# Kernel tuning notes

Hardware: AMD Instinct MI355X
Metric: run time of the kernel (lower is better)

The kernel has to match this reference:

```python
import jax, jax.numpy as jnp
import numpy as np

N_DIMS = 4
NEG_SLOPE = 0.01
ALPHA = 0.5

def leaky(v):
    return jnp.where(v > 0, v, NEG_SLOPE * v)

def gcn_conv(h, W, b, edge_index, n):
    """PyG GCNConv: add self-loops, symmetric normalization, then aggregate."""
    hw = h @ W  # [N, H]
    loops = jnp.arange(n, dtype=edge_index.dtype)
    src = jnp.concatenate([edge_index[0], loops])
    dst = jnp.concatenate([edge_index[1], loops])
    deg = jax.ops.segment_sum(jnp.ones_like(dst, dtype=hw.dtype), dst, num_segments=n)
    dinv = jnp.where(deg > 0, jax.lax.rsqrt(deg), 0.0)
    norm = dinv[src] * dinv[dst]  # [E+N]
    out = jax.ops.segment_sum(hw[src] * norm[:, None], dst, num_segments=n)
    return out + b

def setup_inputs() -> dict:
    key = jax.random.key(0)
    ks = jax.random.split(key, 8)
    N, IN, H, OUT, E = 50000, 512, 256, 512, 800000
    def kaiming(k, shape, fan_in):
        bound = np.sqrt(6.0 / fan_in)  # kaiming_uniform a=sqrt(5)-ish approx; gain sqrt(2)/sqrt(fan_in)*sqrt(3)
        bound = np.sqrt(2.0) * np.sqrt(3.0 / fan_in)
        return jax.random.uniform(k, shape, jnp.float32, -bound, bound)
    x = jax.random.normal(ks[0], (N, IN), jnp.float32)
    all_dim_edge_index = jax.random.randint(ks[1], (N_DIMS, 2, E), 0, N, jnp.int64)
    proj_mat = kaiming(ks[2], (N_DIMS, IN, H), IN)
    gcn_W = jax.random.uniform(ks[3], (N_DIMS, H, H), jnp.float32, -1, 1) * np.sqrt(1.0 / H)
    gcn_b = jnp.zeros((N_DIMS, H), jnp.float32)
    bilinear = kaiming(ks[4], (H, H), H)
    fan = H * N_DIMS
    inv_W = jax.random.uniform(ks[5], (fan, OUT), jnp.float32, -np.sqrt(1.0 / fan), np.sqrt(1.0 / fan))
    inv_b = jax.random.uniform(ks[6], (OUT,), jnp.float32, -np.sqrt(1.0 / fan), np.sqrt(1.0 / fan))
    return {"x": x, "all_dim_edge_index": all_dim_edge_index, "proj_mat": proj_mat,
            "gcn_W": gcn_W, "gcn_b": gcn_b, "bilinear": bilinear, "inv_W": inv_W, "inv_b": inv_b}

def reference(x, all_dim_edge_index, proj_mat, gcn_W, gcn_b, bilinear, inv_W, inv_b):
    n = x.shape[0]
    # per-dimension projection: [n_dims, N, H]
    dim_repr = leaky(jnp.einsum('ni,dih->dnh', x, proj_mat))
    # within-dimension GCN message passing (loop over small fixed n_dims)
    within_aggr = jnp.stack([
        gcn_conv(dim_repr[d], gcn_W[d], gcn_b[d], all_dim_edge_index[d], n)
        for d in range(N_DIMS)])
    # cross-dimension attention
    attention = jnp.einsum('aji,ik,bjk->ab', proj_mat, bilinear, proj_mat)
    attention = jax.nn.softmax(attention, axis=0)
    across_aggr = jnp.einsum('ab,anh->bnh', attention, dim_repr)
    new_dim_repr = ALPHA * within_aggr + (1.0 - ALPHA) * across_aggr  # [n_dims, N, H]
    concat = jnp.transpose(new_dim_repr, (1, 0, 2)).reshape(n, -1)  # [N, n_dims*H]
    return leaky(concat @ inv_W + inv_b)
```

## Files before the change

### kernel.cpp

```cpp
#include <hip/hip_runtime.h>
#include <math.h>

constexpr int N_NODES = 50000;
constexpr int IN_F    = 512;
constexpr int H_F     = 256;
constexpr int OUT_F   = 512;
constexpr int N_EDGE  = 800000;
constexpr int NDIM    = 4;
constexpr long NH     = (long)N_NODES * H_F;

#define LEAKY_SLOPE 0.01f

__device__ __forceinline__ float leaky_f(float v) { return v > 0.0f ? v : LEAKY_SLOPE * v; }

typedef __bf16 bf16x8 __attribute__((ext_vector_type(8)));
typedef float  f32x4  __attribute__((ext_vector_type(4)));

__global__ __launch_bounds__(256) void mfma_gemm_kernel(
    const float* __restrict__ A1, const float* __restrict__ A2, int kSplit,
    const __bf16* __restrict__ BhT, const __bf16* __restrict__ BlT,
    float* __restrict__ C,
    int M, int N, int K, int lda1, int lda2, int ldc,
    int accumulate, int leaky)
{
  __shared__ __bf16 Ash[128][40];
  __shared__ __bf16 Asl[128][40];
  __shared__ __bf16 Bsh[128][40];
  __shared__ __bf16 Bsl[128][40];

  const int tid  = threadIdx.x;
  const int wid  = tid >> 6;
  const int lane = tid & 63;
  const int wm   = wid & 1;
  const int wn   = wid >> 1;
  const int row0 = blockIdx.x * 128;
  const int col0 = blockIdx.y * 128;
  const int l15  = lane & 15;
  const int quad = lane >> 4;

  const int sAm = tid >> 3;
  const int sAk = (tid & 7) * 4;
  const int sBn = tid >> 2;
  const int sBk = (tid & 3) * 8;

  f32x4 acc[4][4] = {};

  const int nkt = K >> 5;
  for (int kt = 0; kt < nkt; ++kt) {
    const float* Asrc; int lda; int k0;
    if (kt * 32 < kSplit) { Asrc = A1; lda = lda1; k0 = kt * 32; }
    else                  { Asrc = A2; lda = lda2; k0 = kt * 32 - kSplit; }

    __syncthreads();
    #pragma unroll
    for (int p = 0; p < 4; ++p) {
      int m = sAm + p * 32;
      int row = row0 + m;
      row = row < M ? row : M - 1;
      float4 v = *(const float4*)(Asrc + (long)row * lda + k0 + sAk);
      float f[4] = {v.x, v.y, v.z, v.w};
      union { __bf16 b[4]; short4 s; } h, l;
      #pragma unroll
      for (int i = 0; i < 4; ++i) {
        __bf16 hb = (__bf16)f[i];
        h.b[i] = hb;
        l.b[i] = (__bf16)(f[i] - (float)hb);
      }
      *(short4*)&Ash[m][sAk] = h.s;
      *(short4*)&Asl[m][sAk] = l.s;
    }
    #pragma unroll
    for (int p = 0; p < 2; ++p) {
      int n = sBn + p * 64;
      long off = (long)(col0 + n) * K + kt * 32 + sBk;
      *(int4*)&Bsh[n][sBk] = *(const int4*)(BhT + off);
      *(int4*)&Bsl[n][sBk] = *(const int4*)(BlT + off);
    }
    __syncthreads();

    bf16x8 ah[4], al[4], bh[4], bl[4];
    #pragma unroll
    for (int t = 0; t < 4; ++t) {
      ah[t] = *(const bf16x8*)&Ash[wm * 64 + t * 16 + l15][quad * 8];
      al[t] = *(const bf16x8*)&Asl[wm * 64 + t * 16 + l15][quad * 8];
      bh[t] = *(const bf16x8*)&Bsh[wn * 64 + t * 16 + l15][quad * 8];
      bl[t] = *(const bf16x8*)&Bsl[wn * 64 + t * 16 + l15][quad * 8];
    }
    #pragma unroll
    for (int mt = 0; mt < 4; ++mt)
      #pragma unroll
      for (int nt = 0; nt < 4; ++nt) {
        acc[mt][nt] = __builtin_amdgcn_mfma_f32_16x16x32_bf16(ah[mt], bh[nt], acc[mt][nt], 0, 0, 0);
        acc[mt][nt] = __builtin_amdgcn_mfma_f32_16x16x32_bf16(ah[mt], bl[nt], acc[mt][nt], 0, 0, 0);
        acc[mt][nt] = __builtin_amdgcn_mfma_f32_16x16x32_bf16(al[mt], bh[nt], acc[mt][nt], 0, 0, 0);
      }
  }

  #pragma unroll
  for (int mt = 0; mt < 4; ++mt)
    #pragma unroll
    for (int nt = 0; nt < 4; ++nt) {
      int col = col0 + wn * 64 + nt * 16 + l15;
      #pragma unroll
      for (int r = 0; r < 4; ++r) {
        int row = row0 + wm * 64 + mt * 16 + quad * 4 + r;
        if (row < M) {
          float* cp = C + (long)row * ldc + col;
          float v = acc[mt][nt][r];
          if (accumulate) v += *cp;
          if (leaky) v = leaky_f(v);
          *cp = v;
        }
      }
    }
}

__global__ __launch_bounds__(256) void sgemm_kernel(
    const float* __restrict__ A, const float* __restrict__ B, float* __restrict__ C,
    int M, int N, int K, int lda, int ldb, int ldc)
{
  __shared__ float As[16][68];
  __shared__ float Bs[16][68];
  const int tid = threadIdx.x;
  const int tx  = tid & 15;
  const int ty  = tid >> 4;
  const int row0 = blockIdx.x * 64;
  const int col0 = blockIdx.y * 64;
  const int mA = tid >> 2;
  const int kA = (tid & 3) * 4;
  const int kB = tid >> 4;
  const int nB = (tid & 15) * 4;
  const int  rowA   = row0 + mA;
  const bool aValid = rowA < M;
  const long aRowOff = (long)rowA * lda;
  float acc[4][4] = {};
  for (int k0 = 0; k0 < K; k0 += 16) {
    float4 av = make_float4(0.f, 0.f, 0.f, 0.f);
    if (aValid) av = *(const float4*)(A + aRowOff + k0 + kA);
    As[kA + 0][mA] = av.x; As[kA + 1][mA] = av.y;
    As[kA + 2][mA] = av.z; As[kA + 3][mA] = av.w;
    float4 bv = *(const float4*)(B + (long)(k0 + kB) * ldb + col0 + nB);
    *(float4*)&Bs[kB][nB] = bv;
    __syncthreads();
    #pragma unroll
    for (int k = 0; k < 16; ++k) {
      float4 a4 = *(const float4*)&As[k][ty * 4];
      float4 b4 = *(const float4*)&Bs[k][tx * 4];
      float ar[4] = {a4.x, a4.y, a4.z, a4.w};
      float br[4] = {b4.x, b4.y, b4.z, b4.w};
      #pragma unroll
      for (int i = 0; i < 4; ++i)
        #pragma unroll
        for (int j = 0; j < 4; ++j)
          acc[i][j] = fmaf(ar[i], br[j], acc[i][j]);
    }
    __syncthreads();
  }
  #pragma unroll
  for (int i = 0; i < 4; ++i) {
    int r = row0 + ty * 4 + i;
    if (r < M)
      *(float4*)(C + (long)r * ldc + col0 + tx * 4) =
          make_float4(acc[i][0], acc[i][1], acc[i][2], acc[i][3]);
  }
}

__global__ void splitT_kernel(const float* __restrict__ B, __bf16* __restrict__ h,
                              __bf16* __restrict__ l, int Kd, int Nd, int total)
{
  int i = blockIdx.x * 256 + threadIdx.x;
  if (i >= total) return;
  int z   = i / (Kd * Nd);
  int rem = i - z * (Kd * Nd);
  int k = rem / Nd;
  int n = rem - k * Nd;
  float v = B[i];
  __bf16 hv = (__bf16)v;
  long o = (long)z * Kd * Nd + (long)n * Kd + k;
  h[o] = hv;
  l[o] = (__bf16)(v - (float)hv);
}

__global__ void bcat_kernel(const float* __restrict__ invW, const float* __restrict__ att,
                            __bf16* __restrict__ h, __bf16* __restrict__ l)
{
  int i = blockIdx.x * 256 + threadIdx.x;
  if (i >= NDIM * OUT_F * 512) return;
  int d   = i >> 18;
  int rem = i & 262143;
  int n = rem >> 9;
  int k = rem & 511;
  float v;
  if (k < H_F) {
    v = invW[(long)(d * H_F + k) * OUT_F + n];
  } else {
    float s = 0.f;
    #pragma unroll
    for (int b = 0; b < 4; ++b)
      s += att[d * 4 + b] * invW[(long)(b * H_F + (k - H_F)) * OUT_F + n];
    v = 0.5f * s;
  }
  __bf16 hv = (__bf16)v;
  h[i] = hv;
  l[i] = (__bf16)(v - (float)hv);
}

__global__ void deg_count_kernel(const int* __restrict__ edges, int* __restrict__ cnt, int E)
{
  int i = blockIdx.x * 256 + threadIdx.x;
  if (i >= NDIM * E) return;
  int d = i / E;
  int e = i - d * E;
  int t = edges[(long)d * 2 * E + E + e];
  atomicAdd(&cnt[d * N_NODES + t], 1);
}

__global__ __launch_bounds__(1024) void scan_kernel(const int* __restrict__ cnt,
                                                    int* __restrict__ row_start,
                                                    float* __restrict__ dinv)
{
  const int d    = blockIdx.x;
  const int tid  = threadIdx.x;
  const int lane = tid & 63;
  const int wid  = tid >> 6;
  __shared__ int wsum[16];
  __shared__ int carry_s;
  if (tid == 0) carry_s = 0;
  __syncthreads();
  for (int base = 0; base < N_NODES; base += 1024) {
    int i = base + tid;
    int v = (i < N_NODES) ? cnt[d * N_NODES + i] : 0;
    if (i < N_NODES) dinv[d * N_NODES + i] = sqrtf(0.5f / (float)(v + 1));
    int incl = v;
    #pragma unroll
    for (int off = 1; off < 64; off <<= 1) {
      int nb = __shfl_up(incl, off, 64);
      if (lane >= off) incl += nb;
    }
    if (lane == 63) wsum[wid] = incl;
    __syncthreads();
    if (wid == 0 && lane < 16) {
      int s = wsum[lane];
      #pragma unroll
      for (int off = 1; off < 16; off <<= 1) {
        int nb = __shfl_up(s, off, 16);
        if (lane >= off) s += nb;
      }
      wsum[lane] = s;
    }
    __syncthreads();
    int waveoff = (wid == 0) ? 0 : wsum[wid - 1];
    if (i < N_NODES) row_start[d * (N_NODES + 1) + i] = carry_s + waveoff + incl - v;
    __syncthreads();
    if (tid == 1023) carry_s += wsum[15];
    __syncthreads();
  }
  if (tid == 0) row_start[d * (N_NODES + 1) + N_NODES] = carry_s;
}

__global__ void fill_kernel(const int* __restrict__ edges, const int* __restrict__ row_start,
                            int* __restrict__ fill_cnt, int* __restrict__ csr_src, int E)
{
  int i = blockIdx.x * 256 + threadIdx.x;
  if (i >= NDIM * E) return;
  int d = i / E;
  int e = i - d * E;
  int s = edges[(long)d * 2 * E + e];
  int t = edges[(long)d * 2 * E + E + e];
  int pos = row_start[d * (N_NODES + 1) + t] + atomicAdd(&fill_cnt[d * N_NODES + t], 1);
  csr_src[(long)d * E + pos] = s;
}

__global__ __launch_bounds__(256) void gather_aggr_kernel(
    const float* __restrict__ hw, const int* __restrict__ csr_src,
    const int* __restrict__ row_start, const float* __restrict__ dinv,
    const float* __restrict__ bias, float* __restrict__ wb)
{
  int n = blockIdx.x * 4 + (threadIdx.x >> 6);
  int lane = threadIdx.x & 63;
  float dt = dinv[n];
  float sl = dt * dt;
  float4 b = *(const float4*)(bias + lane * 4);
  float4 h = *(const float4*)(hw + (long)n * H_F + lane * 4);
  float4 acc = make_float4(0.5f * b.x + sl * h.x, 0.5f * b.y + sl * h.y,
                           0.5f * b.z + sl * h.z, 0.5f * b.w + sl * h.w);
  int beg = row_start[n];
  int end = row_start[n + 1];
  for (int j = beg; j < end; ++j) {
    int s = csr_src[j];
    float nm = dt * dinv[s];
    float4 v = *(const float4*)(hw + (long)s * H_F + lane * 4);
    acc.x = fmaf(nm, v.x, acc.x);
    acc.y = fmaf(nm, v.y, acc.y);
    acc.z = fmaf(nm, v.z, acc.z);
    acc.w = fmaf(nm, v.w, acc.w);
  }
  *(float4*)(wb + (long)n * H_F + lane * 4) = acc;
}

__global__ void att_dot_kernel(const float* __restrict__ T, const float* __restrict__ P,
                               float* __restrict__ out16)
{
  const int a = blockIdx.x >> 2;
  const int b = blockIdx.x & 3;
  const float* ta = T + (long)a * (IN_F * H_F);
  const float* pb = P + (long)b * (IN_F * H_F);
  float s = 0.f;
  for (int i = threadIdx.x; i < IN_F * H_F; i += 256) s += ta[i] * pb[i];
  #pragma unroll
  for (int off = 32; off > 0; off >>= 1) s += __shfl_down(s, off, 64);
  __shared__ float red[4];
  if ((threadIdx.x & 63) == 0) red[threadIdx.x >> 6] = s;
  __syncthreads();
  if (threadIdx.x == 0) out16[blockIdx.x] = red[0] + red[1] + red[2] + red[3];
}

__global__ void att_softmax_kernel(const float* __restrict__ raw, float* __restrict__ att)
{
  int b = threadIdx.x;
  if (b < 4) {
    float r0 = raw[b], r1 = raw[4 + b], r2 = raw[8 + b], r3 = raw[12 + b];
    float m = fmaxf(fmaxf(r0, r1), fmaxf(r2, r3));
    float e0 = expf(r0 - m), e1 = expf(r1 - m), e2 = expf(r2 - m), e3 = expf(r3 - m);
    float inv = 1.0f / (e0 + e1 + e2 + e3);
    att[b] = e0 * inv; att[4 + b] = e1 * inv; att[8 + b] = e2 * inv; att[12 + b] = e3 * inv;
  }
}

__global__ void init_out_kernel(float* __restrict__ out, const float* __restrict__ invB)
{
  long i = (long)blockIdx.x * 256 + threadIdx.x;
  if (i < (long)N_NODES * OUT_F) out[i] = invB[i & (OUT_F - 1)];
}

extern "C" void kernel_launch(void* const* d_in, const int* in_sizes, int n_in,
                              void* d_out, int out_size, void* d_ws, size_t ws_size,
                              hipStream_t stream)
{
  const float* x     = (const float*)d_in[0];
  const int*   edges = (const int*)d_in[1];
  const float* proj  = (const float*)d_in[2];
  const float* gcnW  = (const float*)d_in[3];
  const float* gcnB  = (const float*)d_in[4];
  const float* bil   = (const float*)d_in[5];
  const float* invW  = (const float*)d_in[6];
  const float* invB  = (const float*)d_in[7];
  float* out = (float*)d_out;

  float* R         = (float*)d_ws;
  float* HWB       = R + NH;
  float* WB        = HWB + NH;
  float* dinv      = WB + NH;
  float* Tbuf      = dinv + NDIM * N_NODES;
  float* att_raw   = Tbuf + (long)NDIM * IN_F * H_F;
  float* att       = att_raw + 16;
  int*   cnt       = (int*)(att + 16);
  int*   fill_cnt  = cnt + NDIM * N_NODES;
  int*   row_start = fill_cnt + NDIM * N_NODES;
  int*   csr_src   = row_start + NDIM * (N_NODES + 1);
  __bf16* projTh   = (__bf16*)(csr_src + (long)NDIM * N_EDGE);
  __bf16* projTl   = projTh + (long)NDIM * IN_F * H_F;
  __bf16* gcnWTh   = projTl + (long)NDIM * IN_F * H_F;
  __bf16* gcnWTl   = gcnWTh + (long)NDIM * H_F * H_F;
  __bf16* bcatTh   = gcnWTl + (long)NDIM * H_F * H_F;
  __bf16* bcatTl   = bcatTh + (long)NDIM * OUT_F * 512;

  const int MBL = (N_NODES + 127) / 128;

  hipMemsetAsync(cnt, 0, (size_t)2 * NDIM * N_NODES * sizeof(int), stream);
  deg_count_kernel<<<(NDIM * N_EDGE + 255) / 256, 256, 0, stream>>>(edges, cnt, N_EDGE);
  scan_kernel<<<NDIM, 1024, 0, stream>>>(cnt, row_start, dinv);
  fill_kernel<<<(NDIM * N_EDGE + 255) / 256, 256, 0, stream>>>(edges, row_start, fill_cnt,
                                                               csr_src, N_EDGE);

  splitT_kernel<<<(NDIM * IN_F * H_F + 255) / 256, 256, 0, stream>>>(
      proj, projTh, projTl, IN_F, H_F, NDIM * IN_F * H_F);
  splitT_kernel<<<(NDIM * H_F * H_F + 255) / 256, 256, 0, stream>>>(
      gcnW, gcnWTh, gcnWTl, H_F, H_F, NDIM * H_F * H_F);

  for (int a = 0; a < NDIM; ++a)
    sgemm_kernel<<<dim3(IN_F / 64, H_F / 64, 1), 256, 0, stream>>>(
        proj + (long)a * IN_F * H_F, bil, Tbuf + (long)a * IN_F * H_F,
        IN_F, H_F, H_F, H_F, H_F, H_F);
  att_dot_kernel<<<16, 256, 0, stream>>>(Tbuf, proj, att_raw);
  att_softmax_kernel<<<1, 64, 0, stream>>>(att_raw, att);
  bcat_kernel<<<(NDIM * OUT_F * 512 + 255) / 256, 256, 0, stream>>>(invW, att, bcatTh, bcatTl);

  init_out_kernel<<<(int)(((long)N_NODES * OUT_F + 255) / 256), 256, 0, stream>>>(out, invB);

  for (int d = 0; d < NDIM; ++d) {
    mfma_gemm_kernel<<<dim3(MBL, 2), 256, 0, stream>>>(
        x, x, IN_F, projTh + (long)d * IN_F * H_F, projTl + (long)d * IN_F * H_F, R,
        N_NODES, H_F, IN_F, IN_F, IN_F, H_F, 0, 1);
    mfma_gemm_kernel<<<dim3(MBL, 2), 256, 0, stream>>>(
        R, R, H_F, gcnWTh + (long)d * H_F * H_F, gcnWTl + (long)d * H_F * H_F, HWB,
        N_NODES, H_F, H_F, H_F, H_F, H_F, 0, 0);
    gather_aggr_kernel<<<(N_NODES + 3) / 4, 256, 0, stream>>>(
        HWB, csr_src + (long)d * N_EDGE, row_start + d * (N_NODES + 1),
        dinv + d * N_NODES, gcnB + d * H_F, WB);
    mfma_gemm_kernel<<<dim3(MBL, 4), 256, 0, stream>>>(
        WB, R, H_F, bcatTh + (long)d * OUT_F * 512, bcatTl + (long)d * OUT_F * 512, out,
        N_NODES, OUT_F, 512, H_F, H_F, OUT_F, 1, (d == NDIM - 1) ? 1 : 0);
  }

  (void)in_sizes; (void)n_in; (void)out_size; (void)ws_size;
}
```

Before: 2.530 ms.

## Pre-split activations to bf16 hi/lo and stream GEMM tiles via global_load_lds

Intermediate activations (R, WB, and optionally x) are now stored as bf16 hi/lo pairs, produced in GEMM epilogues and the gather kernel. Later GEMMs can then load their tiles straight into LDS with global_load_lds instead of converting fp32 on every tile load. The change also folds the bias into the first output GEMM, which removes init_out, and moves the attention sgemm onto the MFMA kernel. The gather loop is unrolled by two, and the grid is reordered so column blocks vary fastest. The costs are an extra pass to split x and larger workspace, and the LDS padding is removed, so bank conflicts may increase.

```diff
diff --git a/kernel.cpp b/kernel.cpp
--- a/kernel.cpp
+++ b/kernel.cpp
@@ -16,65 +16,82 @@
 typedef __bf16 bf16x8 __attribute__((ext_vector_type(8)));
 typedef float  f32x4  __attribute__((ext_vector_type(4)));
 
-__global__ __launch_bounds__(256) void mfma_gemm_kernel(
-    const float* __restrict__ A1, const float* __restrict__ A2, int kSplit,
+__device__ __forceinline__ void gload16(const void* g, void* s) {
+  __builtin_amdgcn_global_load_lds(
+      (const __attribute__((address_space(1))) void*)g,
+      (__attribute__((address_space(3))) void*)s, 16, 0, 0);
+}
+
+template<bool AF32>
+__global__ __launch_bounds__(256) void gemm_k(
+    const float* __restrict__ Af, int ldaf,
+    const __bf16* __restrict__ A1h, const __bf16* __restrict__ A1l, int lda1,
+    const __bf16* __restrict__ A2h, const __bf16* __restrict__ A2l, int lda2, int kSplit,
     const __bf16* __restrict__ BhT, const __bf16* __restrict__ BlT,
-    float* __restrict__ C,
-    int M, int N, int K, int lda1, int lda2, int ldc,
-    int accumulate, int leaky)
-{
-  __shared__ __bf16 Ash[128][40];
-  __shared__ __bf16 Asl[128][40];
-  __shared__ __bf16 Bsh[128][40];
-  __shared__ __bf16 Bsl[128][40];
+    float* __restrict__ C, int ldc,
+    const float* __restrict__ biasVec,
+    __bf16* __restrict__ Oh, __bf16* __restrict__ Ol, int ldo,
+    int M, int N, int K, int accumulate, int leaky)
+{
+  __shared__ __bf16 Ash[128][32];
+  __shared__ __bf16 Asl[128][32];
+  __shared__ __bf16 Bsh[128][32];
+  __shared__ __bf16 Bsl[128][32];
 
   const int tid  = threadIdx.x;
+  const int lane = tid & 63;
   const int wid  = tid >> 6;
-  const int lane = tid & 63;
   const int wm   = wid & 1;
   const int wn   = wid >> 1;
-  const int row0 = blockIdx.x * 128;
-  const int col0 = blockIdx.y * 128;
   const int l15  = lane & 15;
   const int quad = lane >> 4;
-
-  const int sAm = tid >> 3;
-  const int sAk = (tid & 7) * 4;
-  const int sBn = tid >> 2;
-  const int sBk = (tid & 3) * 8;
+  const int col0 = blockIdx.x * 128;
+  const int row0 = blockIdx.y * 128;
 
   f32x4 acc[4][4] = {};
-
   const int nkt = K >> 5;
+
   for (int kt = 0; kt < nkt; ++kt) {
-    const float* Asrc; int lda; int k0;
-    if (kt * 32 < kSplit) { Asrc = A1; lda = lda1; k0 = kt * 32; }
-    else                  { Asrc = A2; lda = lda2; k0 = kt * 32 - kSplit; }
-
-    __syncthreads();
-    #pragma unroll
-    for (int p = 0; p < 4; ++p) {
-      int m = sAm + p * 32;
-      int row = row0 + m;
-      row = row < M ? row : M - 1;
-      float4 v = *(const float4*)(Asrc + (long)row * lda + k0 + sAk);
-      float f[4] = {v.x, v.y, v.z, v.w};
-      union { __bf16 b[4]; short4 s; } h, l;
+    const int kk = kt << 5;
+    __syncthreads();
+
+    if constexpr (AF32) {
       #pragma unroll
-      for (int i = 0; i < 4; ++i) {
-        __bf16 hb = (__bf16)f[i];
-        h.b[i] = hb;
-        l.b[i] = (__bf16)(f[i] - (float)hb);
+      for (int p = 0; p < 4; ++p) {
+        const int m = (tid >> 3) + p * 32;
+        int row = row0 + m; row = row < M ? row : M - 1;
+        const float4 v = *(const float4*)(Af + (size_t)row * ldaf + kk + (tid & 7) * 4);
+        const float f[4] = {v.x, v.y, v.z, v.w};
+        union { __bf16 b[4]; short4 s; } hh, ll;
+        #pragma unroll
+        for (int i = 0; i < 4; ++i) {
+          const __bf16 hb = (__bf16)f[i];
+          hh.b[i] = hb;
+          ll.b[i] = (__bf16)(f[i] - (float)hb);
+        }
+        *(short4*)&Ash[m][(tid & 7) * 4] = hh.s;
+        *(short4*)&Asl[m][(tid & 7) * 4] = ll.s;
       }
-      *(short4*)&Ash[m][sAk] = h.s;
-      *(short4*)&Asl[m][sAk] = l.s;
+    } else {
+      const __bf16* Ah; const __bf16* Al; int lda, k0;
+      if (kk < kSplit) { Ah = A1h; Al = A1l; lda = lda1; k0 = kk; }
+      else             { Ah = A2h; Al = A2l; lda = lda2; k0 = kk - kSplit; }
+      #pragma unroll
+      for (int p = 0; p < 2; ++p) {
+        const int c = tid + p * 256;
+        int row = row0 + (c >> 2); row = row < M ? row : M - 1;
+        const size_t go = (size_t)row * lda + k0 + (c & 3) * 8;
+        gload16(Ah + go, (__bf16*)Ash + (size_t)c * 8);
+        gload16(Al + go, (__bf16*)Asl + (size_t)c * 8);
+      }
     }
     #pragma unroll
     for (int p = 0; p < 2; ++p) {
-      int n = sBn + p * 64;
-      long off = (long)(col0 + n) * K + kt * 32 + sBk;
-      *(int4*)&Bsh[n][sBk] = *(const int4*)(BhT + off);
-      *(int4*)&Bsl[n][sBk] = *(const int4*)(BlT + off);
+      const int c = tid + p * 256;
+      const int nn = col0 + (c >> 2);
+      const size_t go = (size_t)nn * K + kk + (c & 3) * 8;
+      gload16(BhT + go, (__bf16*)Bsh + (size_t)c * 8);
+      gload16(BlT + go, (__bf16*)Bsl + (size_t)c * 8);
     }
     __syncthreads();
 
@@ -100,69 +117,25 @@
   for (int mt = 0; mt < 4; ++mt)
     #pragma unroll
     for (int nt = 0; nt < 4; ++nt) {
-      int col = col0 + wn * 64 + nt * 16 + l15;
+      const int col = col0 + wn * 64 + nt * 16 + l15;
+      const float bv = biasVec ? biasVec[col] : 0.0f;
       #pragma unroll
       for (int r = 0; r < 4; ++r) {
-        int row = row0 + wm * 64 + mt * 16 + quad * 4 + r;
+        const int row = row0 + wm * 64 + mt * 16 + quad * 4 + r;
         if (row < M) {
-          float* cp = C + (long)row * ldc + col;
-          float v = acc[mt][nt][r];
-          if (accumulate) v += *cp;
+          float v = acc[mt][nt][r] + bv;
+          if (accumulate) v += C[(size_t)row * ldc + col];
           if (leaky) v = leaky_f(v);
-          *cp = v;
+          if (Oh) {
+            const __bf16 hv = (__bf16)v;
+            Oh[(size_t)row * ldo + col] = hv;
+            Ol[(size_t)row * ldo + col] = (__bf16)(v - (float)hv);
+          } else {
+            C[(size_t)row * ldc + col] = v;
+          }
         }
       }
     }
-}
-
-__global__ __launch_bounds__(256) void sgemm_kernel(
-    const float* __restrict__ A, const float* __restrict__ B, float* __restrict__ C,
-    int M, int N, int K, int lda, int ldb, int ldc)
-{
-  __shared__ float As[16][68];
-  __shared__ float Bs[16][68];
-  const int tid = threadIdx.x;
-  const int tx  = tid & 15;
-  const int ty  = tid >> 4;
-  const int row0 = blockIdx.x * 64;
-  const int col0 = blockIdx.y * 64;
-  const int mA = tid >> 2;
-  const int kA = (tid & 3) * 4;
-  const int kB = tid >> 4;
-  const int nB = (tid & 15) * 4;
-  const int  rowA   = row0 + mA;
-  const bool aValid = rowA < M;
-  const long aRowOff = (long)rowA * lda;
-  float acc[4][4] = {};
-  for (int k0 = 0; k0 < K; k0 += 16) {
-    float4 av = make_float4(0.f, 0.f, 0.f, 0.f);
-    if (aValid) av = *(const float4*)(A + aRowOff + k0 + kA);
-    As[kA + 0][mA] = av.x; As[kA + 1][mA] = av.y;
-    As[kA + 2][mA] = av.z; As[kA + 3][mA] = av.w;
-    float4 bv = *(const float4*)(B + (long)(k0 + kB) * ldb + col0 + nB);
-    *(float4*)&Bs[kB][nB] = bv;
-    __syncthreads();
-    #pragma unroll
-    for (int k = 0; k < 16; ++k) {
-      float4 a4 = *(const float4*)&As[k][ty * 4];
-      float4 b4 = *(const float4*)&Bs[k][tx * 4];
-      float ar[4] = {a4.x, a4.y, a4.z, a4.w};
-      float br[4] = {b4.x, b4.y, b4.z, b4.w};
-      #pragma unroll
-      for (int i = 0; i < 4; ++i)
-        #pragma unroll
-        for (int j = 0; j < 4; ++j)
-          acc[i][j] = fmaf(ar[i], br[j], acc[i][j]);
-    }
-    __syncthreads();
-  }
-  #pragma unroll
-  for (int i = 0; i < 4; ++i) {
-    int r = row0 + ty * 4 + i;
-    if (r < M)
-      *(float4*)(C + (long)r * ldc + col0 + tx * 4) =
-          make_float4(acc[i][0], acc[i][1], acc[i][2], acc[i][3]);
-  }
 }
 
 __global__ void splitT_kernel(const float* __restrict__ B, __bf16* __restrict__ h,
@@ -179,6 +152,17 @@
   long o = (long)z * Kd * Nd + (long)n * Kd + k;
   h[o] = hv;
   l[o] = (__bf16)(v - (float)hv);
+}
+
+__global__ void splitA_kernel(const float* __restrict__ A, __bf16* __restrict__ h,
+                              __bf16* __restrict__ l, long total)
+{
+  long i = (long)blockIdx.x * 256 + threadIdx.x;
+  if (i >= total) return;
+  float v = A[i];
+  __bf16 hv = (__bf16)v;
+  h[i] = hv;
+  l[i] = (__bf16)(v - (float)hv);
 }
 
 __global__ void bcat_kernel(const float* __restrict__ invW, const float* __restrict__ att,
@@ -274,28 +258,49 @@
 __global__ __launch_bounds__(256) void gather_aggr_kernel(
     const float* __restrict__ hw, const int* __restrict__ csr_src,
     const int* __restrict__ row_start, const float* __restrict__ dinv,
-    const float* __restrict__ bias, float* __restrict__ wb)
-{
-  int n = blockIdx.x * 4 + (threadIdx.x >> 6);
-  int lane = threadIdx.x & 63;
-  float dt = dinv[n];
-  float sl = dt * dt;
-  float4 b = *(const float4*)(bias + lane * 4);
-  float4 h = *(const float4*)(hw + (long)n * H_F + lane * 4);
-  float4 acc = make_float4(0.5f * b.x + sl * h.x, 0.5f * b.y + sl * h.y,
-                           0.5f * b.z + sl * h.z, 0.5f * b.w + sl * h.w);
-  int beg = row_start[n];
-  int end = row_start[n + 1];
-  for (int j = beg; j < end; ++j) {
-    int s = csr_src[j];
-    float nm = dt * dinv[s];
-    float4 v = *(const float4*)(hw + (long)s * H_F + lane * 4);
-    acc.x = fmaf(nm, v.x, acc.x);
-    acc.y = fmaf(nm, v.y, acc.y);
-    acc.z = fmaf(nm, v.z, acc.z);
-    acc.w = fmaf(nm, v.w, acc.w);
-  }
-  *(float4*)(wb + (long)n * H_F + lane * 4) = acc;
+    const float* __restrict__ bias, __bf16* __restrict__ Wh, __bf16* __restrict__ Wl)
+{
+  const int n = blockIdx.x * 4 + (threadIdx.x >> 6);
+  const int lane = threadIdx.x & 63;
+  const float dt = dinv[n];
+  const float sl = dt * dt;
+  const float4 b = *(const float4*)(bias + lane * 4);
+  const float4 h = *(const float4*)(hw + (size_t)n * H_F + lane * 4);
+  float4 a0 = make_float4(0.5f * b.x + sl * h.x, 0.5f * b.y + sl * h.y,
+                          0.5f * b.z + sl * h.z, 0.5f * b.w + sl * h.w);
+  float4 a1 = make_float4(0.f, 0.f, 0.f, 0.f);
+  const int beg = row_start[n];
+  const int end = row_start[n + 1];
+  int j = beg;
+  for (; j + 2 <= end; j += 2) {
+    const int s0 = csr_src[j];
+    const int s1 = csr_src[j + 1];
+    const float nm0 = dt * dinv[s0];
+    const float nm1 = dt * dinv[s1];
+    const float4 v0 = *(const float4*)(hw + (size_t)s0 * H_F + lane * 4);
+    const float4 v1 = *(const float4*)(hw + (size_t)s1 * H_F + lane * 4);
+    a0.x = fmaf(nm0, v0.x, a0.x); a0.y = fmaf(nm0, v0.y, a0.y);
+    a0.z = fmaf(nm0, v0.z, a0.z); a0.w = fmaf(nm0, v0.w, a0.w);
+    a1.x = fmaf(nm1, v1.x, a1.x); a1.y = fmaf(nm1, v1.y, a1.y);
+    a1.z = fmaf(nm1, v1.z, a1.z); a1.w = fmaf(nm1, v1.w, a1.w);
+  }
+  if (j < end) {
+    const int s0 = csr_src[j];
+    const float nm0 = dt * dinv[s0];
+    const float4 v0 = *(const float4*)(hw + (size_t)s0 * H_F + lane * 4);
+    a0.x = fmaf(nm0, v0.x, a0.x); a0.y = fmaf(nm0, v0.y, a0.y);
+    a0.z = fmaf(nm0, v0.z, a0.z); a0.w = fmaf(nm0, v0.w, a0.w);
+  }
+  const float av[4] = {a0.x + a1.x, a0.y + a1.y, a0.z + a1.z, a0.w + a1.w};
+  union { __bf16 b[4]; short4 s; } H, L;
+  #pragma unroll
+  for (int i = 0; i < 4; ++i) {
+    const __bf16 hv = (__bf16)av[i];
+    H.b[i] = hv;
+    L.b[i] = (__bf16)(av[i] - (float)hv);
+  }
+  *(short4*)(Wh + (size_t)n * H_F + lane * 4) = H.s;
+  *(short4*)(Wl + (size_t)n * H_F + lane * 4) = L.s;
 }
 
 __global__ void att_dot_kernel(const float* __restrict__ T, const float* __restrict__ P,
@@ -327,12 +332,6 @@
   }
 }
 
-__global__ void init_out_kernel(float* __restrict__ out, const float* __restrict__ invB)
-{
-  long i = (long)blockIdx.x * 256 + threadIdx.x;
-  if (i < (long)N_NODES * OUT_F) out[i] = invB[i & (OUT_F - 1)];
-}
-
 extern "C" void kernel_launch(void* const* d_in, const int* in_sizes, int n_in,
                               void* d_out, int out_size, void* d_ws, size_t ws_size,
                               hipStream_t stream)
@@ -347,10 +346,8 @@
   const float* invB  = (const float*)d_in[7];
   float* out = (float*)d_out;
 
-  float* R         = (float*)d_ws;
-  float* HWB       = R + NH;
-  float* WB        = HWB + NH;
-  float* dinv      = WB + NH;
+  float* HWB       = (float*)d_ws;
+  float* dinv      = HWB + NH;
   float* Tbuf      = dinv + NDIM * N_NODES;
   float* att_raw   = Tbuf + (long)NDIM * IN_F * H_F;
   float* att       = att_raw + 16;
@@ -364,6 +361,16 @@
   __bf16* gcnWTl   = gcnWTh + (long)NDIM * H_F * H_F;
   __bf16* bcatTh   = gcnWTl + (long)NDIM * H_F * H_F;
   __bf16* bcatTl   = bcatTh + (long)NDIM * OUT_F * 512;
+  __bf16* bilTh    = bcatTl + (long)NDIM * OUT_F * 512;
+  __bf16* bilTl    = bilTh + (long)H_F * H_F;
+  __bf16* Rh       = bilTl + (long)H_F * H_F;
+  __bf16* Rl       = Rh + NH;
+  __bf16* WBh      = Rl + NH;
+  __bf16* WBl      = WBh + NH;
+  __bf16* xh       = WBl + NH;
+  __bf16* xl       = xh + (long)N_NODES * IN_F;
+  const size_t need_x = (size_t)((char*)(xl + (long)N_NODES * IN_F) - (char*)d_ws);
+  const bool XS = ws_size >= need_x;
 
   const int MBL = (N_NODES + 127) / 128;
 
@@ -377,30 +384,62 @@
       proj, projTh, projTl, IN_F, H_F, NDIM * IN_F * H_F);
   splitT_kernel<<<(NDIM * H_F * H_F + 255) / 256, 256, 0, stream>>>(
       gcnW, gcnWTh, gcnWTl, H_F, H_F, NDIM * H_F * H_F);
+  splitT_kernel<<<(H_F * H_F + 255) / 256, 256, 0, stream>>>(
+      bil, bilTh, bilTl, H_F, H_F, H_F * H_F);
 
   for (int a = 0; a < NDIM; ++a)
-    sgemm_kernel<<<dim3(IN_F / 64, H_F / 64, 1), 256, 0, stream>>>(
-        proj + (long)a * IN_F * H_F, bil, Tbuf + (long)a * IN_F * H_F,
-        IN_F, H_F, H_F, H_F, H_F, H_F);
+    gemm_k<true><<<dim3(H_F / 128, IN_F / 128), 256, 0, stream>>>(
+        proj + (long)a * IN_F * H_F, H_F,
+        nullptr, nullptr, 0, nullptr, nullptr, 0, 0,
+        bilTh, bilTl,
+        Tbuf + (long)a * IN_F * H_F, H_F,
+        nullptr, nullptr, nullptr, 0,
+        IN_F, H_F, H_F, 0, 0);
   att_dot_kernel<<<16, 256, 0, stream>>>(Tbuf, proj, att_raw);
   att_softmax_kernel<<<1, 64, 0, stream>>>(att_raw, att);
   bcat_kernel<<<(NDIM * OUT_F * 512 + 255) / 256, 256, 0, stream>>>(invW, att, bcatTh, bcatTl);
 
-  init_out_kernel<<<(int)(((long)N_NODES * OUT_F + 255) / 256), 256, 0, stream>>>(out, invB);
+  if (XS)
+    splitA_kernel<<<(int)(((long)N_NODES * IN_F + 255) / 256), 256, 0, stream>>>(
+        x, xh, xl, (long)N_NODES * IN_F);
 
   for (int d = 0; d < NDIM; ++d) {
-    mfma_gemm_kernel<<<dim3(MBL, 2), 256, 0, stream>>>(
-        x, x, IN_F, projTh + (long)d * IN_F * H_F, projTl + (long)d * IN_F * H_F, R,
-        N_NODES, H_F, IN_F, IN_F, IN_F, H_F, 0, 1);
-    mfma_gemm_kernel<<<dim3(MBL, 2), 256, 0, stream>>>(
-        R, R, H_F, gcnWTh + (long)d * H_F * H_F, gcnWTl + (long)d * H_F * H_F, HWB,
-        N_NODES, H_F, H_F, H_F, H_F, H_F, 0, 0);
-    gather_aggr_kernel<<<(N_NODES + 3) / 4, 256, 0, stream>>>(
+    if (XS)
+      gemm_k<false><<<dim3(H_F / 128, MBL), 256, 0, stream>>>(
+          nullptr, 0,
+          xh, xl, IN_F, xh, xl, IN_F, IN_F,
+          projTh + (long)d * IN_F * H_F, projTl + (long)d * IN_F * H_F,
+          nullptr, 0, nullptr,
+          Rh, Rl, H_F,
+          N_NODES, H_F, IN_F, 0, 1);
+    else
+      gemm_k<true><<<dim3(H_F / 128, MBL), 256, 0, stream>>>(
+          x, IN_F,
+          nullptr, nullptr, 0, nullptr, nullptr, 0, 0,
+          projTh + (long)d * IN_F * H_F, projTl + (long)d * IN_F * H_F,
+          nullptr, 0, nullptr,
+          Rh, Rl, H_F,
+          N_NODES, H_F, IN_F, 0, 1);
+
+    gemm_k<false><<<dim3(H_F / 128, MBL), 256, 0, stream>>>(
+        nullptr, 0,
+        Rh, Rl, H_F, Rh, Rl, H_F, H_F,
+        gcnWTh + (long)d * H_F * H_F, gcnWTl + (long)d * H_F * H_F,
+        HWB, H_F, nullptr,
+        nullptr, nullptr, 0,
+        N_NODES, H_F, H_F, 0, 0);
+
+    gather_aggr_kernel<<<N_NODES / 4, 256, 0, stream>>>(
         HWB, csr_src + (long)d * N_EDGE, row_start + d * (N_NODES + 1),
-        dinv + d * N_NODES, gcnB + d * H_F, WB);
-    mfma_gemm_kernel<<<dim3(MBL, 4), 256, 0, stream>>>(
-        WB, R, H_F, bcatTh + (long)d * OUT_F * 512, bcatTl + (long)d * OUT_F * 512, out,
-        N_NODES, OUT_F, 512, H_F, H_F, OUT_F, 1, (d == NDIM - 1) ? 1 : 0);
+        dinv + d * N_NODES, gcnB + d * H_F, WBh, WBl);
+
+    gemm_k<false><<<dim3(OUT_F / 128, MBL), 256, 0, stream>>>(
+        nullptr, 0,
+        WBh, WBl, H_F, Rh, Rl, H_F, H_F,
+        bcatTh + (long)d * OUT_F * 512, bcatTl + (long)d * OUT_F * 512,
+        out, OUT_F, (d == 0) ? invB : nullptr,
+        nullptr, nullptr, 0,
+        N_NODES, OUT_F, 512, (d == 0) ? 0 : 1, (d == NDIM - 1) ? 1 : 0);
   }
 
   (void)in_sizes; (void)n_in; (void)out_size; (void)ws_size;
```

Result: slower. 2.927 ms (+15.7%).
